# Optimization experiments

Hardware: AMD Instinct MI355X
Metric: run time of the kernel (lower is better)

The kernel has to match this reference:

```python
import jax, jax.numpy as jnp
import numpy as np

N = 100000   # nodes
E = 625000   # edges
D = 128      # feature / embedding dim
C = 40       # num classes
BN_EPS = 1e-5
L2_EPS = 1e-12


def setup_inputs() -> dict:
    key = jax.random.key(0)
    ks = jax.random.split(key, 8)
    s = 1.0 / np.sqrt(D)
    return {
        "x": jax.random.normal(ks[0], (N, D), dtype=jnp.float32),
        "edge_index": jax.random.randint(ks[1], (2, E), 0, N, dtype=jnp.int64),
        "W1": jax.random.normal(ks[2], (D, D), dtype=jnp.float32) * s,
        "b1": jnp.zeros((D,), jnp.float32),
        "W2": jax.random.normal(ks[3], (D, D), dtype=jnp.float32) * s,
        "b2": jnp.zeros((D,), jnp.float32),
        "W3": jax.random.normal(ks[4], (D, D), dtype=jnp.float32) * s,
        "b3": jnp.zeros((D,), jnp.float32),
        "g1": jnp.ones((D,), jnp.float32), "be1": jnp.zeros((D,), jnp.float32),
        "g2": jnp.ones((D,), jnp.float32), "be2": jnp.zeros((D,), jnp.float32),
        "g3": jnp.ones((D,), jnp.float32), "be3": jnp.zeros((D,), jnp.float32),
        "Wout": jax.random.normal(ks[5], (D, C), dtype=jnp.float32) * s,
        "bout": jnp.zeros((C,), jnp.float32),
    }


def _gcn_norm(edge_index, n):
    # PyG GCNConv default: add self loops, symmetric normalization
    loop = jnp.arange(n)
    src = jnp.concatenate([edge_index[0], loop])
    dst = jnp.concatenate([edge_index[1], loop])
    deg = jax.ops.segment_sum(jnp.ones_like(src, dtype=jnp.float32), dst, num_segments=n)
    dinv = jnp.where(deg > 0, jax.lax.rsqrt(deg), 0.0)
    norm = dinv[src] * dinv[dst]  # [E+N]
    return src, dst, norm


def _gcn_conv(x, W, b, src, dst, norm, n):
    h = x @ W                                # [N, D]
    msg = h[src] * norm[:, None]             # gather, [E+N, D]
    out = jax.ops.segment_sum(msg, dst, num_segments=n)  # scatter-add
    return out + b


def _bn(x, g, b):
    mu = jnp.mean(x, axis=0)
    var = jnp.var(x, axis=0)
    return (x - mu) * jax.lax.rsqrt(var + BN_EPS) * g + b


def _l2norm(x):
    n = jnp.sqrt(jnp.sum(x * x, axis=1, keepdims=True))
    return x / jnp.maximum(n, L2_EPS)


def reference(x, edge_index, W1, b1, W2, b2, W3, b3,
              g1, be1, g2, be2, g3, be3, Wout, bout):
    n = x.shape[0]
    src, dst, norm = _gcn_norm(edge_index, n)

    h = jax.nn.relu(_bn(_gcn_conv(x, W1, b1, src, dst, norm, n), g1, be1))
    h = _l2norm(h)
    r = h
    h = jax.nn.relu(_bn(_gcn_conv(h, W2, b2, src, dst, norm, n), g2, be2))
    h = _l2norm(h + r)
    r = h
    h = jax.nn.relu(_bn(_gcn_conv(h, W3, b3, src, dst, norm, n), g3, be3))
    h = _l2norm(h + r)

    return h @ Wout + bout  # node classification logits [N, C]
```

## Files before the change

### kernel.cpp

```cpp
#include <hip/hip_runtime.h>
#include <math.h>

#define DD 128
#define COUT 40
#define BN_EPS 1e-5f
#define L2_EPS 1e-12f
#define NREP 64

typedef __attribute__((ext_vector_type(8))) short bf16x8;
typedef __attribute__((ext_vector_type(4))) float f32x4;
typedef __attribute__((ext_vector_type(4))) unsigned int u32x4;

static __device__ inline unsigned short f2bf(float f) {
    unsigned int x = __float_as_uint(f);
    unsigned int r = (x + 0x7FFFu + ((x >> 16) & 1u)) >> 16;
    return (unsigned short)r;
}
static __device__ inline float bf2f(unsigned short u) {
    return __uint_as_float(((unsigned int)u) << 16);
}


__global__ void k_hist(const int* __restrict__ ei, int E, int* __restrict__ deg,
                       int* __restrict__ pord) {
    int i = blockIdx.x * blockDim.x + threadIdx.x;
    if (i < E) pord[i] = atomicAdd(&deg[ei[E + i]], 1);
}

__global__ void k_scan_a(const int* __restrict__ deg, int* __restrict__ row_ptr,
                         int* __restrict__ bsum, float* __restrict__ dinv, int n) {
    __shared__ int s[256];
    int t = threadIdx.x;
    int idx = blockIdx.x * 256 + t;
    int v = (idx < n) ? deg[idx] : 0;
    if (idx < n) dinv[idx] = rsqrtf((float)(v + 1));
    s[t] = v; __syncthreads();
    for (int off = 1; off < 256; off <<= 1) {
        int x = (t >= off) ? s[t - off] : 0;
        __syncthreads(); s[t] += x; __syncthreads();
    }
    if (idx <= n) row_ptr[idx] = s[t] - v;
    if (t == 255) bsum[blockIdx.x] = s[255];
}

__global__ void k_scan_b(const int* __restrict__ bsum, int* __restrict__ boff, int nb) {
    __shared__ int s[512];
    int t = threadIdx.x;
    int v = (t < nb) ? bsum[t] : 0;
    s[t] = v; __syncthreads();
    for (int off = 1; off < 512; off <<= 1) {
        int x = (t >= off) ? s[t - off] : 0;
        __syncthreads(); s[t] += x; __syncthreads();
    }
    if (t < nb) boff[t] = s[t] - v;
}

__global__ void k_fill(const int* __restrict__ ei, const int* __restrict__ pord,
                       int E, const int* __restrict__ row_ptr,
                       const int* __restrict__ boff, int* __restrict__ perm) {
    int i = blockIdx.x * blockDim.x + threadIdx.x;
    if (i >= E) return;
    int u = ei[i];
    int v = ei[E + i];
    int pos = row_ptr[v] + boff[v >> 8] + pord[i];
    perm[pos] = u;
}

__global__ void k_wrepack_all(const float* __restrict__ W1, const float* __restrict__ W2,
                              const float* __restrict__ W3, const float* __restrict__ Wout,
                              unsigned short* __restrict__ wb,
                              unsigned short* __restrict__ wob,
                              float* __restrict__ stats,
                              int* __restrict__ deg, int n) {
    int b = blockIdx.x;
    if (b < 24) {
        int wi = b >> 3;
        const float* W = (wi == 0) ? W1 : (wi == 1) ? W2 : W3;
        unsigned short* out = wb + wi * 16384;
        int idx = (b & 7) * 256 + threadIdx.x;
        int kc = idx >> 9;
        int cc = (idx >> 6) & 7;
        int lane = idx & 63;
        int nn = cc * 16 + (lane & 15);
        int kb = kc * 32 + (lane >> 4) * 8;
        unsigned short tmp[8];
#pragma unroll
        for (int j = 0; j < 8; j++) tmp[j] = f2bf(W[(size_t)(kb + j) * DD + nn]);
        *(uint4*)&out[(size_t)idx * 8] = *(const uint4*)tmp;
    } else if (b < 27) {
        int idx = (b - 24) * 256 + threadIdx.x;
        int kc = idx / 192;
        int rem = idx % 192;
        int cc = rem >> 6;
        int lane = rem & 63;
        int nn = cc * 16 + (lane & 15);
        int kb = kc * 32 + (lane >> 4) * 8;
        unsigned short tmp[8];
#pragma unroll
        for (int j = 0; j < 8; j++)
            tmp[j] = (nn < COUT) ? f2bf(Wout[(size_t)(kb + j) * COUT + nn]) : 0;
        *(uint4*)&wob[(size_t)idx * 8] = *(const uint4*)tmp;
    } else {
        int idx = (b - 27) * 256 + threadIdx.x;
        float4 z = make_float4(0.f, 0.f, 0.f, 0.f);
        for (int i = idx; i < 3 * NREP * 64; i += 8 * 256)
            ((float4*)stats)[i] = z;
        int4 iz = make_int4(0, 0, 0, 0);
        for (int i = idx; i < (n >> 2); i += 8 * 256)
            ((int4*)deg)[i] = iz;
        if (b == 27 && threadIdx.x < (n & 3)) deg[(n & ~3) + threadIdx.x] = 0;
    }
}


__global__ __launch_bounds__(256) void k_gemm0(const float* __restrict__ A,
                                               const unsigned short* __restrict__ Wb,
                                               const float* __restrict__ dinv,
                                               unsigned short* __restrict__ C, int nrows) {
    __shared__ __align__(16) unsigned short Ws[16384];
    const int tid = threadIdx.x;
    for (int i = tid; i < 2048; i += 256)
        ((uint4*)Ws)[i] = ((const uint4*)Wb)[i];
    __syncthreads();

    const int wv = tid >> 6;
    const int lane = tid & 63;
    const int R0 = blockIdx.x * 64 + wv * 16;
    if (R0 >= nrows) return;
    const int m = lane & 15, q = lane >> 4;
    int rr = R0 + m; if (rr >= nrows) rr = nrows - 1;
    const float* Ar = A + (size_t)rr * DD + q * 8;

    bf16x8 af[4];
#pragma unroll
    for (int kc = 0; kc < 4; kc++) {
        float4 lo = *(const float4*)(Ar + kc * 32);
        float4 hi = *(const float4*)(Ar + kc * 32 + 4);
        unsigned short t[8];
        t[0] = f2bf(lo.x); t[1] = f2bf(lo.y); t[2] = f2bf(lo.z); t[3] = f2bf(lo.w);
        t[4] = f2bf(hi.x); t[5] = f2bf(hi.y); t[6] = f2bf(hi.z); t[7] = f2bf(hi.w);
        af[kc] = *(const bf16x8*)t;
    }

    f32x4 acc[8];
#pragma unroll
    for (int cc = 0; cc < 8; cc++) acc[cc] = (f32x4){0.f, 0.f, 0.f, 0.f};
#pragma unroll
    for (int kc = 0; kc < 4; kc++)
#pragma unroll
        for (int cc = 0; cc < 8; cc++) {
            bf16x8 b = *(const bf16x8*)&Ws[(size_t)((kc * 8 + cc) * 64 + lane) * 8];
            acc[cc] = __builtin_amdgcn_mfma_f32_16x16x32_bf16(af[kc], b, acc[cc], 0, 0, 0);
        }

    float dr[4];
#pragma unroll
    for (int i = 0; i < 4; i++) {
        int r = R0 + q * 4 + i;
        dr[i] = (r < nrows) ? dinv[r] : 0.f;
    }
#pragma unroll
    for (int cc = 0; cc < 8; cc++)
#pragma unroll
        for (int i = 0; i < 4; i++) {
            int r = R0 + q * 4 + i;
            if (r < nrows) C[(size_t)r * DD + cc * 16 + m] = f2bf(acc[cc][i] * dr[i]);
        }
}

__global__ __launch_bounds__(256) void k_aggs(const unsigned short* __restrict__ lin,
                                              const int* __restrict__ row_ptr,
                                              const int* __restrict__ boff,
                                              const int* __restrict__ perm,
                                              const float* __restrict__ dinv,
                                              const float* __restrict__ bias,
                                              unsigned short* __restrict__ outb,
                                              float* __restrict__ stats, int n) {
    const int tid = threadIdx.x;
    const int wv = tid >> 6;
    const int lane = tid & 63;
    const int half = lane >> 5;
    const int li = lane & 31;
    const int slot = li >> 4;
    const int ci = (li & 15) * 8;

    const int v = blockIdx.x * 8 + wv * 2 + half;
    const bool valid = v < n;

    float acc[8];
#pragma unroll
    for (int k = 0; k < 8; k++) acc[k] = 0.f;
    float dv = 0.f;

    if (valid) {
        const int s0 = row_ptr[v] + boff[v >> 8];
        const int e0 = row_ptr[v + 1] + boff[(v + 1) >> 8];
        dv = dinv[v];
        if (slot == 0) {
            uint4 t = *(const uint4*)&lin[(size_t)v * DD + ci];
            acc[0] = __uint_as_float(t.x << 16);
            acc[1] = __uint_as_float(t.x & 0xFFFF0000u);
            acc[2] = __uint_as_float(t.y << 16);
            acc[3] = __uint_as_float(t.y & 0xFFFF0000u);
            acc[4] = __uint_as_float(t.z << 16);
            acc[5] = __uint_as_float(t.z & 0xFFFF0000u);
            acc[6] = __uint_as_float(t.w << 16);
            acc[7] = __uint_as_float(t.w & 0xFFFF0000u);
        }
        for (int j = s0; j < e0; j += 8) {
            int i0 = j + slot;
            int i1 = j + 2 + slot;
            int i2 = j + 4 + slot;
            int i3 = j + 6 + slot;
            bool b0 = i0 < e0, b1 = i1 < e0, b2 = i2 < e0, b3 = i3 < e0;
            int u0, u1, u2, u3;
            if (b0) u0 = perm[i0];
            if (b1) u1 = perm[i1];
            if (b2) u2 = perm[i2];
            if (b3) u3 = perm[i3];
            uint4 t0, t1, t2, t3;
            if (b0) t0 = *(const uint4*)&lin[(size_t)u0 * DD + ci];
            if (b1) t1 = *(const uint4*)&lin[(size_t)u1 * DD + ci];
            if (b2) t2 = *(const uint4*)&lin[(size_t)u2 * DD + ci];
            if (b3) t3 = *(const uint4*)&lin[(size_t)u3 * DD + ci];
            if (b0) {
                acc[0] += __uint_as_float(t0.x << 16);
                acc[1] += __uint_as_float(t0.x & 0xFFFF0000u);
                acc[2] += __uint_as_float(t0.y << 16);
                acc[3] += __uint_as_float(t0.y & 0xFFFF0000u);
                acc[4] += __uint_as_float(t0.z << 16);
                acc[5] += __uint_as_float(t0.z & 0xFFFF0000u);
                acc[6] += __uint_as_float(t0.w << 16);
                acc[7] += __uint_as_float(t0.w & 0xFFFF0000u);
            }
            if (b1) {
                acc[0] += __uint_as_float(t1.x << 16);
                acc[1] += __uint_as_float(t1.x & 0xFFFF0000u);
                acc[2] += __uint_as_float(t1.y << 16);
                acc[3] += __uint_as_float(t1.y & 0xFFFF0000u);
                acc[4] += __uint_as_float(t1.z << 16);
                acc[5] += __uint_as_float(t1.z & 0xFFFF0000u);
                acc[6] += __uint_as_float(t1.w << 16);
                acc[7] += __uint_as_float(t1.w & 0xFFFF0000u);
            }
            if (b2) {
                acc[0] += __uint_as_float(t2.x << 16);
                acc[1] += __uint_as_float(t2.x & 0xFFFF0000u);
                acc[2] += __uint_as_float(t2.y << 16);
                acc[3] += __uint_as_float(t2.y & 0xFFFF0000u);
                acc[4] += __uint_as_float(t2.z << 16);
                acc[5] += __uint_as_float(t2.z & 0xFFFF0000u);
                acc[6] += __uint_as_float(t2.w << 16);
                acc[7] += __uint_as_float(t2.w & 0xFFFF0000u);
            }
            if (b3) {
                acc[0] += __uint_as_float(t3.x << 16);
                acc[1] += __uint_as_float(t3.x & 0xFFFF0000u);
                acc[2] += __uint_as_float(t3.y << 16);
                acc[3] += __uint_as_float(t3.y & 0xFFFF0000u);
                acc[4] += __uint_as_float(t3.z << 16);
                acc[5] += __uint_as_float(t3.z & 0xFFFF0000u);
                acc[6] += __uint_as_float(t3.w << 16);
                acc[7] += __uint_as_float(t3.w & 0xFFFF0000u);
            }
        }
    }
#pragma unroll
    for (int k = 0; k < 8; k++) acc[k] += __shfl_xor(acc[k], 16, 64);

    __shared__ float sh[8][128];
    __shared__ float qh[8][128];
    const int prow = wv * 2 + half;
    if (slot == 0) {
        if (valid) {
            float4 bb0 = *(const float4*)&bias[ci];
            float4 bb1 = *(const float4*)&bias[ci + 4];
            float bs[8] = {bb0.x, bb0.y, bb0.z, bb0.w, bb1.x, bb1.y, bb1.z, bb1.w};
            unsigned short t[8];
#pragma unroll
            for (int k = 0; k < 8; k++) {
                float a = acc[k] * dv + bs[k];
                t[k] = f2bf(a);
                sh[prow][ci + k] = a;
                qh[prow][ci + k] = a * a;
            }
            *(uint4*)&outb[(size_t)v * DD + ci] = *(const uint4*)t;
        } else {
#pragma unroll
            for (int k = 0; k < 8; k++) { sh[prow][ci + k] = 0.f; qh[prow][ci + k] = 0.f; }
        }
    }
    __syncthreads();
    if (tid < 128) {
        float a = 0.f, b = 0.f;
#pragma unroll
        for (int g = 0; g < 8; g++) { a += sh[g][tid]; b += qh[g][tid]; }
        float* st = stats + (size_t)(blockIdx.x & (NREP - 1)) * 256;
        atomicAdd(&st[tid], a);
        atomicAdd(&st[128 + tid], b);
    }
}

template <bool HAS_RES>
__global__ __launch_bounds__(256) void k_fused(const unsigned short* __restrict__ aggX,
                                               const float* __restrict__ stats,
                                               const float* __restrict__ g,
                                               const float* __restrict__ be, float inv_n,
                                               const unsigned short* __restrict__ resb,
                                               const unsigned short* __restrict__ Wb,
                                               const float* __restrict__ dinv,
                                               unsigned short* __restrict__ hbf_out,
                                               unsigned short* __restrict__ linb_out,
                                               int nrows) {
    __shared__ __align__(16) unsigned short Ws[16384];
    __shared__ float ssl[256];
    const int tid = threadIdx.x;
    for (int i = tid; i < 2048; i += 256)
        ((uint4*)Ws)[i] = ((const uint4*)Wb)[i];
    if (tid < 128) {
        float sa = 0.f, sb = 0.f;
        for (int r = 0; r < NREP; r++) {
            sa += stats[r * 256 + tid];
            sb += stats[r * 256 + 128 + tid];
        }
        float mu = sa * inv_n;
        float var = sb * inv_n - mu * mu;
        float sc = g[tid] * rsqrtf(var + BN_EPS);
        ssl[tid] = sc;
        ssl[128 + tid] = be[tid] - mu * sc;
    }
    __syncthreads();

    const int wv = tid >> 6;
    const int lane = tid & 63;
    const int R0 = blockIdx.x * 64 + wv * 16;
    if (R0 >= nrows) return;
    const int m = lane & 15, q = lane >> 4;
    int rr = R0 + m; if (rr >= nrows) rr = nrows - 1;
    const unsigned short* Ar = aggX + (size_t)rr * DD + q * 8;
    const unsigned short* Rr = HAS_RES ? resb + (size_t)rr * DD + q * 8 : nullptr;

    float y[4][8];
    float sq = 0.f;
#pragma unroll
    for (int kc = 0; kc < 4; kc++) {
        ushort4 lo = *(const ushort4*)(Ar + kc * 32);
        ushort4 hi = *(const ushort4*)(Ar + kc * 32 + 4);
        unsigned short av[8] = {lo.x, lo.y, lo.z, lo.w, hi.x, hi.y, hi.z, hi.w};
        int c0 = kc * 32 + q * 8;
        float4 sc0 = *(const float4*)&ssl[c0];
        float4 sc1 = *(const float4*)&ssl[c0 + 4];
        float4 sh0 = *(const float4*)&ssl[128 + c0];
        float4 sh1 = *(const float4*)&ssl[128 + c0 + 4];
        float scv[8] = {sc0.x, sc0.y, sc0.z, sc0.w, sc1.x, sc1.y, sc1.z, sc1.w};
        float shv[8] = {sh0.x, sh0.y, sh0.z, sh0.w, sh1.x, sh1.y, sh1.z, sh1.w};
        if (HAS_RES) {
            ushort4 rl = *(const ushort4*)(Rr + kc * 32);
            ushort4 rh = *(const ushort4*)(Rr + kc * 32 + 4);
            unsigned short rv[8] = {rl.x, rl.y, rl.z, rl.w, rh.x, rh.y, rh.z, rh.w};
#pragma unroll
            for (int j = 0; j < 8; j++) {
                float yy = fmaxf(bf2f(av[j]) * scv[j] + shv[j], 0.f) + bf2f(rv[j]);
                y[kc][j] = yy; sq += yy * yy;
            }
        } else {
#pragma unroll
            for (int j = 0; j < 8; j++) {
                float yy = fmaxf(bf2f(av[j]) * scv[j] + shv[j], 0.f);
                y[kc][j] = yy; sq += yy * yy;
            }
        }
    }
    sq += __shfl_xor(sq, 16, 64);
    sq += __shfl_xor(sq, 32, 64);
    float inv = 1.f / fmaxf(sqrtf(sq), L2_EPS);

    bf16x8 af[4];
#pragma unroll
    for (int kc = 0; kc < 4; kc++) {
        unsigned short t[8];
#pragma unroll
        for (int j = 0; j < 8; j++) t[j] = f2bf(y[kc][j] * inv);
        af[kc] = *(const bf16x8*)t;
        *(bf16x8*)&hbf_out[(size_t)rr * DD + q * 8 + kc * 32] = af[kc];
    }

    f32x4 acc[8];
#pragma unroll
    for (int cc = 0; cc < 8; cc++) acc[cc] = (f32x4){0.f, 0.f, 0.f, 0.f};
#pragma unroll
    for (int kc = 0; kc < 4; kc++)
#pragma unroll
        for (int cc = 0; cc < 8; cc++) {
            bf16x8 b = *(const bf16x8*)&Ws[(size_t)((kc * 8 + cc) * 64 + lane) * 8];
            acc[cc] = __builtin_amdgcn_mfma_f32_16x16x32_bf16(af[kc], b, acc[cc], 0, 0, 0);
        }

    float dr[4];
#pragma unroll
    for (int i = 0; i < 4; i++) {
        int r = R0 + q * 4 + i;
        dr[i] = (r < nrows) ? dinv[r] : 0.f;
    }
#pragma unroll
    for (int cc = 0; cc < 8; cc++)
#pragma unroll
        for (int i = 0; i < 4; i++) {
            int r = R0 + q * 4 + i;
            if (r < nrows) linb_out[(size_t)r * DD + cc * 16 + m] = f2bf(acc[cc][i] * dr[i]);
        }
}

__global__ __launch_bounds__(256) void k_outfused(const unsigned short* __restrict__ aggX,
                                                  const float* __restrict__ stats,
                                                  const float* __restrict__ g,
                                                  const float* __restrict__ be, float inv_n,
                                                  const unsigned short* __restrict__ resb,
                                                  const unsigned short* __restrict__ wob,
                                                  const float* __restrict__ bout,
                                                  float* __restrict__ C, int nrows) {
    __shared__ __align__(16) unsigned short Ws[6144];
    __shared__ float ssl[256];
    const int tid = threadIdx.x;
    for (int i = tid; i < 768; i += 256)
        ((uint4*)Ws)[i] = ((const uint4*)wob)[i];
    if (tid < 128) {
        float sa = 0.f, sb = 0.f;
        for (int r = 0; r < NREP; r++) {
            sa += stats[r * 256 + tid];
            sb += stats[r * 256 + 128 + tid];
        }
        float mu = sa * inv_n;
        float var = sb * inv_n - mu * mu;
        float sc = g[tid] * rsqrtf(var + BN_EPS);
        ssl[tid] = sc;
        ssl[128 + tid] = be[tid] - mu * sc;
    }
    __syncthreads();

    const int wv = tid >> 6;
    const int lane = tid & 63;
    const int R0 = blockIdx.x * 64 + wv * 16;
    if (R0 >= nrows) return;
    const int m = lane & 15, q = lane >> 4;
    int rr = R0 + m; if (rr >= nrows) rr = nrows - 1;
    const unsigned short* Ar = aggX + (size_t)rr * DD + q * 8;
    const unsigned short* Rr = resb + (size_t)rr * DD + q * 8;

    float y[4][8];
    float sq = 0.f;
#pragma unroll
    for (int kc = 0; kc < 4; kc++) {
        ushort4 lo = *(const ushort4*)(Ar + kc * 32);
        ushort4 hi = *(const ushort4*)(Ar + kc * 32 + 4);
        ushort4 rl = *(const ushort4*)(Rr + kc * 32);
        ushort4 rh = *(const ushort4*)(Rr + kc * 32 + 4);
        unsigned short av[8] = {lo.x, lo.y, lo.z, lo.w, hi.x, hi.y, hi.z, hi.w};
        unsigned short rv[8] = {rl.x, rl.y, rl.z, rl.w, rh.x, rh.y, rh.z, rh.w};
        int c0 = kc * 32 + q * 8;
        float4 sc0 = *(const float4*)&ssl[c0];
        float4 sc1 = *(const float4*)&ssl[c0 + 4];
        float4 sh0 = *(const float4*)&ssl[128 + c0];
        float4 sh1 = *(const float4*)&ssl[128 + c0 + 4];
        float scv[8] = {sc0.x, sc0.y, sc0.z, sc0.w, sc1.x, sc1.y, sc1.z, sc1.w};
        float shv[8] = {sh0.x, sh0.y, sh0.z, sh0.w, sh1.x, sh1.y, sh1.z, sh1.w};
#pragma unroll
        for (int j = 0; j < 8; j++) {
            float yy = fmaxf(bf2f(av[j]) * scv[j] + shv[j], 0.f) + bf2f(rv[j]);
            y[kc][j] = yy; sq += yy * yy;
        }
    }
    sq += __shfl_xor(sq, 16, 64);
    sq += __shfl_xor(sq, 32, 64);
    float inv = 1.f / fmaxf(sqrtf(sq), L2_EPS);

    bf16x8 af[4];
#pragma unroll
    for (int kc = 0; kc < 4; kc++) {
        unsigned short t[8];
#pragma unroll
        for (int j = 0; j < 8; j++) t[j] = f2bf(y[kc][j] * inv);
        af[kc] = *(const bf16x8*)t;
    }

    f32x4 acc[3];
#pragma unroll
    for (int cc = 0; cc < 3; cc++) acc[cc] = (f32x4){0.f, 0.f, 0.f, 0.f};
#pragma unroll
    for (int kc = 0; kc < 4; kc++)
#pragma unroll
        for (int cc = 0; cc < 3; cc++) {
            bf16x8 b = *(const bf16x8*)&Ws[(size_t)((kc * 3 + cc) * 64 + lane) * 8];
            acc[cc] = __builtin_amdgcn_mfma_f32_16x16x32_bf16(af[kc], b, acc[cc], 0, 0, 0);
        }

#pragma unroll
    for (int cc = 0; cc < 3; cc++) {
        int col = cc * 16 + m;
        if (col < COUT) {
            float bb = bout[col];
#pragma unroll
            for (int i = 0; i < 4; i++) {
                int r = R0 + q * 4 + i;
                if (r < nrows) C[(size_t)r * COUT + col] = acc[cc][i] + bb;
            }
        }
    }
}


extern "C" void kernel_launch(void* const* d_in, const int* in_sizes, int n_in,
                              void* d_out, int out_size, void* d_ws, size_t ws_size,
                              hipStream_t stream) {
    const float* x    = (const float*)d_in[0];
    const int*   ei   = (const int*)d_in[1];
    const float* W1   = (const float*)d_in[2];
    const float* b1   = (const float*)d_in[3];
    const float* W2   = (const float*)d_in[4];
    const float* b2   = (const float*)d_in[5];
    const float* W3   = (const float*)d_in[6];
    const float* b3   = (const float*)d_in[7];
    const float* g1   = (const float*)d_in[8];
    const float* be1  = (const float*)d_in[9];
    const float* g2   = (const float*)d_in[10];
    const float* be2  = (const float*)d_in[11];
    const float* g3   = (const float*)d_in[12];
    const float* be3  = (const float*)d_in[13];
    const float* Wout = (const float*)d_in[14];
    const float* bout = (const float*)d_in[15];
    float* out = (float*)d_out;

    const int N = in_sizes[0] / DD;
    const int E = in_sizes[1] / 2;
    const int SSTRIDE = NREP * 256;

    char* w = (char*)d_ws;
    unsigned short* linb = (unsigned short*)w; w += (size_t)N * DD * sizeof(unsigned short);
    unsigned short* aggA = (unsigned short*)w; w += (size_t)N * DD * sizeof(unsigned short);
    unsigned short* aggB = (unsigned short*)w; w += (size_t)N * DD * sizeof(unsigned short);
    unsigned short* hbf1 = (unsigned short*)w; w += (size_t)N * DD * sizeof(unsigned short);
    unsigned short* hbf2 = (unsigned short*)w; w += (size_t)N * DD * sizeof(unsigned short);
    unsigned short* wb   = (unsigned short*)w; w += 3 * 16384 * sizeof(unsigned short);
    unsigned short* wob  = (unsigned short*)w; w += 6144 * sizeof(unsigned short);
    int* perm    = (int*)w;                    w += (size_t)E * sizeof(int);
    int* pord    = (int*)w;                    w += (size_t)E * sizeof(int);
    int* deg     = (int*)w;                    w += (size_t)N * sizeof(int);
    int* row_ptr = (int*)w;                    w += (size_t)(N + 1) * sizeof(int);
    float* dinv  = (float*)w;                  w += (size_t)N * sizeof(float);
    int* bsum    = (int*)w;                    w += 512 * sizeof(int);
    int* boff    = (int*)w;                    w += 512 * sizeof(int);
    float* stats = (float*)w;                  w += 3 * (size_t)SSTRIDE * sizeof(float);

    const int NB = (N + 1 + 255) / 256;

    k_wrepack_all<<<35, 256, 0, stream>>>(W1, W2, W3, Wout, wb, wob, stats, deg, N);
    k_hist<<<(E + 255) / 256, 256, 0, stream>>>(ei, E, deg, pord);
    k_scan_a<<<NB, 256, 0, stream>>>(deg, row_ptr, bsum, dinv, N);
    k_scan_b<<<1, 512, 0, stream>>>(bsum, boff, NB);
    k_fill<<<(E + 255) / 256, 256, 0, stream>>>(ei, pord, E, row_ptr, boff, perm);

    int gemmGrid = (N + 63) / 64;
    int aggGrid = (N + 7) / 8;
    float inv_n = 1.0f / (float)N;

    k_gemm0<<<gemmGrid, 256, 0, stream>>>(x, wb, dinv, linb, N);
    k_aggs<<<aggGrid, 256, 0, stream>>>(linb, row_ptr, boff, perm, dinv, b1, aggA, stats, N);
    k_fused<false><<<gemmGrid, 256, 0, stream>>>(aggA, stats, g1, be1, inv_n,
                                                 nullptr, wb + 16384, dinv, hbf1, linb, N);
    k_aggs<<<aggGrid, 256, 0, stream>>>(linb, row_ptr, boff, perm, dinv, b2, aggB,
                                        stats + SSTRIDE, N);
    k_fused<true><<<gemmGrid, 256, 0, stream>>>(aggB, stats + SSTRIDE, g2, be2, inv_n,
                                                hbf1, wb + 32768, dinv, hbf2, linb, N);
    k_aggs<<<aggGrid, 256, 0, stream>>>(linb, row_ptr, boff, perm, dinv, b3, aggA,
                                        stats + 2 * SSTRIDE, N);
    k_outfused<<<gemmGrid, 256, 0, stream>>>(aggA, stats + 2 * SSTRIDE, g3, be3, inv_n,
                                             hbf2, wob, bout, out, N);
}
```

Before: 395.6 us.

## Merge setup kernels to cut launches: hist+repack, single-pass scan, fill+gemm0

Folds the histogram into the weight repack kernel and replaces deg zeroing with a memset. The two-pass scan becomes one kernel that uses a last-block ticket counter to compute the block offsets. The CSR fill is merged into the first GEMM launch as extra blocks. This removes several kernel launches and their serialization gaps from the preprocessing. The cost is reliance on atomics and threadfence for the ticket and more complex block indexing. The fill and GEMM blocks share a launch, so the large shared-memory allocation also applies to the fill blocks.

```diff
diff --git a/kernel.cpp b/kernel.cpp
--- a/kernel.cpp
+++ b/kernel.cpp
@@ -9,7 +9,6 @@
 
 typedef __attribute__((ext_vector_type(8))) short bf16x8;
 typedef __attribute__((ext_vector_type(4))) float f32x4;
-typedef __attribute__((ext_vector_type(4))) unsigned int u32x4;
 
 static __device__ inline unsigned short f2bf(float f) {
     unsigned int x = __float_as_uint(f);
@@ -21,58 +20,20 @@
 }
 
 
-__global__ void k_hist(const int* __restrict__ ei, int E, int* __restrict__ deg,
-                       int* __restrict__ pord) {
-    int i = blockIdx.x * blockDim.x + threadIdx.x;
-    if (i < E) pord[i] = atomicAdd(&deg[ei[E + i]], 1);
-}
-
-__global__ void k_scan_a(const int* __restrict__ deg, int* __restrict__ row_ptr,
-                         int* __restrict__ bsum, float* __restrict__ dinv, int n) {
-    __shared__ int s[256];
-    int t = threadIdx.x;
-    int idx = blockIdx.x * 256 + t;
-    int v = (idx < n) ? deg[idx] : 0;
-    if (idx < n) dinv[idx] = rsqrtf((float)(v + 1));
-    s[t] = v; __syncthreads();
-    for (int off = 1; off < 256; off <<= 1) {
-        int x = (t >= off) ? s[t - off] : 0;
-        __syncthreads(); s[t] += x; __syncthreads();
-    }
-    if (idx <= n) row_ptr[idx] = s[t] - v;
-    if (t == 255) bsum[blockIdx.x] = s[255];
-}
-
-__global__ void k_scan_b(const int* __restrict__ bsum, int* __restrict__ boff, int nb) {
-    __shared__ int s[512];
-    int t = threadIdx.x;
-    int v = (t < nb) ? bsum[t] : 0;
-    s[t] = v; __syncthreads();
-    for (int off = 1; off < 512; off <<= 1) {
-        int x = (t >= off) ? s[t - off] : 0;
-        __syncthreads(); s[t] += x; __syncthreads();
-    }
-    if (t < nb) boff[t] = s[t] - v;
-}
-
-__global__ void k_fill(const int* __restrict__ ei, const int* __restrict__ pord,
-                       int E, const int* __restrict__ row_ptr,
-                       const int* __restrict__ boff, int* __restrict__ perm) {
-    int i = blockIdx.x * blockDim.x + threadIdx.x;
-    if (i >= E) return;
-    int u = ei[i];
-    int v = ei[E + i];
-    int pos = row_ptr[v] + boff[v >> 8] + pord[i];
-    perm[pos] = u;
-}
-
-__global__ void k_wrepack_all(const float* __restrict__ W1, const float* __restrict__ W2,
-                              const float* __restrict__ W3, const float* __restrict__ Wout,
-                              unsigned short* __restrict__ wb,
-                              unsigned short* __restrict__ wob,
-                              float* __restrict__ stats,
-                              int* __restrict__ deg, int n) {
-    int b = blockIdx.x;
+__global__ void k_setup1(const int* __restrict__ ei, int E, int* __restrict__ deg,
+                         int* __restrict__ pord,
+                         const float* __restrict__ W1, const float* __restrict__ W2,
+                         const float* __restrict__ W3, const float* __restrict__ Wout,
+                         unsigned short* __restrict__ wb,
+                         unsigned short* __restrict__ wob,
+                         float* __restrict__ stats,
+                         int histGrid) {
+    if ((int)blockIdx.x < histGrid) {
+        int i = blockIdx.x * 256 + threadIdx.x;
+        if (i < E) pord[i] = atomicAdd(&deg[ei[E + i]], 1);
+        return;
+    }
+    int b = blockIdx.x - histGrid;
     if (b < 24) {
         int wi = b >> 3;
         const float* W = (wi == 0) ? W1 : (wi == 1) ? W2 : W3;
@@ -101,31 +62,80 @@
             tmp[j] = (nn < COUT) ? f2bf(Wout[(size_t)(kb + j) * COUT + nn]) : 0;
         *(uint4*)&wob[(size_t)idx * 8] = *(const uint4*)tmp;
     } else {
+        float4 z = make_float4(0.f, 0.f, 0.f, 0.f);
         int idx = (b - 27) * 256 + threadIdx.x;
-        float4 z = make_float4(0.f, 0.f, 0.f, 0.f);
         for (int i = idx; i < 3 * NREP * 64; i += 8 * 256)
             ((float4*)stats)[i] = z;
-        int4 iz = make_int4(0, 0, 0, 0);
-        for (int i = idx; i < (n >> 2); i += 8 * 256)
-            ((int4*)deg)[i] = iz;
-        if (b == 27 && threadIdx.x < (n & 3)) deg[(n & ~3) + threadIdx.x] = 0;
-    }
-}
-
-
-__global__ __launch_bounds__(256) void k_gemm0(const float* __restrict__ A,
-                                               const unsigned short* __restrict__ Wb,
-                                               const float* __restrict__ dinv,
-                                               unsigned short* __restrict__ C, int nrows) {
+    }
+}
+
+__global__ void k_scan(const int* __restrict__ deg, int* __restrict__ row_ptr,
+                       int* __restrict__ bsum, float* __restrict__ dinv,
+                       int* __restrict__ boff, int* __restrict__ cnt, int n) {
+    __shared__ int s[256];
+    __shared__ int tick;
+    int t = threadIdx.x;
+    int idx = blockIdx.x * 256 + t;
+    int v = (idx < n) ? deg[idx] : 0;
+    if (idx < n) dinv[idx] = rsqrtf((float)(v + 1));
+    s[t] = v; __syncthreads();
+    for (int off = 1; off < 256; off <<= 1) {
+        int x = (t >= off) ? s[t - off] : 0;
+        __syncthreads(); s[t] += x; __syncthreads();
+    }
+    if (idx <= n) row_ptr[idx] = s[t] - v;
+    if (t == 255) atomicExch(&bsum[blockIdx.x], s[255]);
+    __threadfence();
+    __syncthreads();
+    if (t == 0) tick = atomicAdd(cnt, 1);
+    __syncthreads();
+    if (tick == (int)gridDim.x - 1) {
+        __threadfence();
+        int nb = gridDim.x;
+        int e0 = (2 * t < nb) ? atomicAdd(&bsum[2 * t], 0) : 0;
+        int e1 = (2 * t + 1 < nb) ? atomicAdd(&bsum[2 * t + 1], 0) : 0;
+        int pair = e0 + e1;
+        s[t] = pair; __syncthreads();
+        for (int off = 1; off < 256; off <<= 1) {
+            int x = (t >= off) ? s[t - off] : 0;
+            __syncthreads(); s[t] += x; __syncthreads();
+        }
+        int pex = s[t] - pair;
+        if (2 * t < nb) boff[2 * t] = pex;
+        if (2 * t + 1 < nb) boff[2 * t + 1] = pex + e0;
+    }
+}
+
+
+__global__ __launch_bounds__(256) void k_gemmfill(const float* __restrict__ A,
+                                                  const unsigned short* __restrict__ Wb,
+                                                  const float* __restrict__ dinv,
+                                                  unsigned short* __restrict__ C, int nrows,
+                                                  const int* __restrict__ ei,
+                                                  const int* __restrict__ pord, int E,
+                                                  const int* __restrict__ row_ptr,
+                                                  const int* __restrict__ boff,
+                                                  int* __restrict__ perm, int fillGrid) {
     __shared__ __align__(16) unsigned short Ws[16384];
     const int tid = threadIdx.x;
+    if ((int)blockIdx.x < fillGrid) {
+        int i = blockIdx.x * 256 + tid;
+        if (i < E) {
+            int u = ei[i];
+            int v = ei[E + i];
+            int pos = row_ptr[v] + boff[v >> 8] + pord[i];
+            perm[pos] = u;
+        }
+        return;
+    }
+    const int bg = blockIdx.x - fillGrid;
     for (int i = tid; i < 2048; i += 256)
         ((uint4*)Ws)[i] = ((const uint4*)Wb)[i];
     __syncthreads();
 
     const int wv = tid >> 6;
     const int lane = tid & 63;
-    const int R0 = blockIdx.x * 64 + wv * 16;
+    const int R0 = bg * 64 + wv * 16;
     if (R0 >= nrows) return;
     const int m = lane & 15, q = lane >> 4;
     int rr = R0 + m; if (rr >= nrows) rr = nrows - 1;
@@ -545,6 +555,7 @@
     int* perm    = (int*)w;                    w += (size_t)E * sizeof(int);
     int* pord    = (int*)w;                    w += (size_t)E * sizeof(int);
     int* deg     = (int*)w;                    w += (size_t)N * sizeof(int);
+    int* cnt     = (int*)w;                    w += 4 * sizeof(int);
     int* row_ptr = (int*)w;                    w += (size_t)(N + 1) * sizeof(int);
     float* dinv  = (float*)w;                  w += (size_t)N * sizeof(float);
     int* bsum    = (int*)w;                    w += 512 * sizeof(int);
@@ -552,18 +563,20 @@
     float* stats = (float*)w;                  w += 3 * (size_t)SSTRIDE * sizeof(float);
 
     const int NB = (N + 1 + 255) / 256;
-
-    k_wrepack_all<<<35, 256, 0, stream>>>(W1, W2, W3, Wout, wb, wob, stats, deg, N);
-    k_hist<<<(E + 255) / 256, 256, 0, stream>>>(ei, E, deg, pord);
-    k_scan_a<<<NB, 256, 0, stream>>>(deg, row_ptr, bsum, dinv, N);
-    k_scan_b<<<1, 512, 0, stream>>>(bsum, boff, NB);
-    k_fill<<<(E + 255) / 256, 256, 0, stream>>>(ei, pord, E, row_ptr, boff, perm);
-
-    int gemmGrid = (N + 63) / 64;
-    int aggGrid = (N + 7) / 8;
-    float inv_n = 1.0f / (float)N;
-
-    k_gemm0<<<gemmGrid, 256, 0, stream>>>(x, wb, dinv, linb, N);
+    const int histGrid = (E + 255) / 256;
+    const int gemmGrid = (N + 63) / 64;
+    const int aggGrid = (N + 7) / 8;
+    const float inv_n = 1.0f / (float)N;
+
+    hipMemsetAsync(deg, 0, ((size_t)N + 4) * sizeof(int), stream);
+    k_setup1<<<histGrid + 35, 256, 0, stream>>>(ei, E, deg, pord,
+                                                W1, W2, W3, Wout, wb, wob, stats, histGrid);
+    k_scan<<<NB, 256, 0, stream>>>(deg, row_ptr, bsum, dinv, boff, cnt, N);
+
+    k_gemmfill<<<histGrid + gemmGrid, 256, 0, stream>>>(x, wb, dinv, linb, N,
+                                                        ei, pord, E, row_ptr, boff,
+                                                        perm, histGrid);
+
     k_aggs<<<aggGrid, 256, 0, stream>>>(linb, row_ptr, boff, perm, dinv, b1, aggA, stats, N);
     k_fused<false><<<gemmGrid, 256, 0, stream>>>(aggA, stats, g1, be1, inv_n,
                                                  nullptr, wb + 16384, dinv, hbf1, linb, N);
```

Result: slower. 413.1 us (+4.4%).

## Split aggregation into two column-half passes with 16 lanes per node

Applied to the files above, without the earlier changes.

The aggregation kernel now splits the 128 feature columns into two halves handled by separate grid halves. Each node gets 16 lanes (two edge slots of 8 lanes) covering 64 columns, and each block covers 16 nodes. The aim is to shrink each pass's gathered working set (64 bf16 columns per row) so it stays in cache, and to raise the number of nodes in flight. In exchange, each edge's index and perm lookups are read twice, each gather moves 128 bytes instead of 256, and the grid doubles in size.

```diff
diff --git a/kernel.cpp b/kernel.cpp
--- a/kernel.cpp
+++ b/kernel.cpp
@@ -9,7 +9,6 @@
 
 typedef __attribute__((ext_vector_type(8))) short bf16x8;
 typedef __attribute__((ext_vector_type(4))) float f32x4;
-typedef __attribute__((ext_vector_type(4))) unsigned int u32x4;
 
 static __device__ inline unsigned short f2bf(float f) {
     unsigned int x = __float_as_uint(f);
@@ -175,16 +174,17 @@
                                               const float* __restrict__ dinv,
                                               const float* __restrict__ bias,
                                               unsigned short* __restrict__ outb,
-                                              float* __restrict__ stats, int n) {
+                                              float* __restrict__ stats, int n,
+                                              int halfGrid) {
     const int tid = threadIdx.x;
-    const int wv = tid >> 6;
-    const int lane = tid & 63;
-    const int half = lane >> 5;
-    const int li = lane & 31;
-    const int slot = li >> 4;
-    const int ci = (li & 15) * 8;
-
-    const int v = blockIdx.x * 8 + wv * 2 + half;
+    const int pass = ((int)blockIdx.x >= halfGrid) ? 1 : 0;
+    const int bg = blockIdx.x - pass * halfGrid;
+    const int grp = tid >> 4;
+    const int li = tid & 15;
+    const int slot = li >> 3;
+    const int ci = pass * 64 + (li & 7) * 8;
+
+    const int v = bg * 16 + grp;
     const bool valid = v < n;
 
     float acc[8];
@@ -266,12 +266,12 @@
         }
     }
 #pragma unroll
-    for (int k = 0; k < 8; k++) acc[k] += __shfl_xor(acc[k], 16, 64);
-
-    __shared__ float sh[8][128];
-    __shared__ float qh[8][128];
-    const int prow = wv * 2 + half;
+    for (int k = 0; k < 8; k++) acc[k] += __shfl_xor(acc[k], 8, 64);
+
+    __shared__ float sh[16][64];
+    __shared__ float qh[16][64];
     if (slot == 0) {
+        const int cl = (li & 7) * 8;
         if (valid) {
             float4 bb0 = *(const float4*)&bias[ci];
             float4 bb1 = *(const float4*)&bias[ci + 4];
@@ -281,23 +281,23 @@
             for (int k = 0; k < 8; k++) {
                 float a = acc[k] * dv + bs[k];
                 t[k] = f2bf(a);
-                sh[prow][ci + k] = a;
-                qh[prow][ci + k] = a * a;
+                sh[grp][cl + k] = a;
+                qh[grp][cl + k] = a * a;
             }
             *(uint4*)&outb[(size_t)v * DD + ci] = *(const uint4*)t;
         } else {
 #pragma unroll
-            for (int k = 0; k < 8; k++) { sh[prow][ci + k] = 0.f; qh[prow][ci + k] = 0.f; }
+            for (int k = 0; k < 8; k++) { sh[grp][cl + k] = 0.f; qh[grp][cl + k] = 0.f; }
         }
     }
     __syncthreads();
-    if (tid < 128) {
+    if (tid < 64) {
         float a = 0.f, b = 0.f;
 #pragma unroll
-        for (int g = 0; g < 8; g++) { a += sh[g][tid]; b += qh[g][tid]; }
+        for (int g = 0; g < 16; g++) { a += sh[g][tid]; b += qh[g][tid]; }
         float* st = stats + (size_t)(blockIdx.x & (NREP - 1)) * 256;
-        atomicAdd(&st[tid], a);
-        atomicAdd(&st[128 + tid], b);
+        atomicAdd(&st[pass * 64 + tid], a);
+        atomicAdd(&st[128 + pass * 64 + tid], b);
     }
 }
 
@@ -559,20 +559,22 @@
     k_scan_b<<<1, 512, 0, stream>>>(bsum, boff, NB);
     k_fill<<<(E + 255) / 256, 256, 0, stream>>>(ei, pord, E, row_ptr, boff, perm);
 
-    int gemmGrid = (N + 63) / 64;
-    int aggGrid = (N + 7) / 8;
-    float inv_n = 1.0f / (float)N;
+    const int gemmGrid = (N + 63) / 64;
+    const int halfGrid = (N + 15) / 16;
+    const int aggGrid = 2 * halfGrid;
+    const float inv_n = 1.0f / (float)N;
 
     k_gemm0<<<gemmGrid, 256, 0, stream>>>(x, wb, dinv, linb, N);
-    k_aggs<<<aggGrid, 256, 0, stream>>>(linb, row_ptr, boff, perm, dinv, b1, aggA, stats, N);
+    k_aggs<<<aggGrid, 256, 0, stream>>>(linb, row_ptr, boff, perm, dinv, b1, aggA,
+                                        stats, N, halfGrid);
     k_fused<false><<<gemmGrid, 256, 0, stream>>>(aggA, stats, g1, be1, inv_n,
                                                  nullptr, wb + 16384, dinv, hbf1, linb, N);
     k_aggs<<<aggGrid, 256, 0, stream>>>(linb, row_ptr, boff, perm, dinv, b2, aggB,
-                                        stats + SSTRIDE, N);
+                                        stats + SSTRIDE, N, halfGrid);
     k_fused<true><<<gemmGrid, 256, 0, stream>>>(aggB, stats + SSTRIDE, g2, be2, inv_n,
                                                 hbf1, wb + 32768, dinv, hbf2, linb, N);
     k_aggs<<<aggGrid, 256, 0, stream>>>(linb, row_ptr, boff, perm, dinv, b3, aggA,
-                                        stats + 2 * SSTRIDE, N);
+                                        stats + 2 * SSTRIDE, N, halfGrid);
     k_outfused<<<gemmGrid, 256, 0, stream>>>(aggA, stats + 2 * SSTRIDE, g3, be3, inv_n,
                                              hbf2, wob, bout, out, N);
 }
```

After: 400.9 us. No clear change (+1.3%).
